# Kernel tuning notes

Hardware: AMD Instinct MI355X
Metric: run time of the kernel (lower is better)

## Reference

```python
import jax, jax.numpy as jnp
import numpy as np

B, N, C = 8, 4096, 512

def setup_inputs() -> dict:
    key = jax.random.key(0)
    ks = jax.random.split(key, 6)
    s = 1.0 / np.sqrt(C)
    return {
        "x": jax.random.normal(ks[0], (B, N, C), jnp.float32),
        "Wq": jax.random.normal(ks[1], (C, C), jnp.float32) * s,
        "Wk": jax.random.normal(ks[2], (C, C), jnp.float32) * s,
        "Wv": jax.random.normal(ks[3], (C, C), jnp.float32) * s,
        "W1": jax.random.normal(ks[4], (C, C), jnp.float32) * s,
        "W2": jax.random.normal(ks[5], (C, C), jnp.float32) * s,
    }

def reference(x, Wq, Wk, Wv, W1, W2):
    # torch nn.Linear: y = x @ W.T (bias=False)
    q = x @ Wq.T                      # [B,N,C]
    k = x @ Wk.T
    v = x @ Wv.T
    dim = q.shape[-1]
    q = jax.nn.softmax(q, axis=-1) * (dim ** -0.5)   # softmax over channels
    k = jax.nn.softmax(k, axis=-2)                   # softmax over sequence
    context = jnp.einsum('bnd,bne->bde', k, v)       # [B,C,C]
    attn = jnp.einsum('bnd,bde->bne', q, context)    # [B,N,C]
    x = attn + x
    return (x @ W1.T) @ W2.T + x
```

## Files before the change

### kernel.cpp

```cpp
#include <hip/hip_runtime.h>

typedef unsigned int uint;
typedef __bf16 bf16_t;
typedef bf16_t bf16x8 __attribute__((ext_vector_type(8)));
typedef float floatx4 __attribute__((ext_vector_type(4)));

struct __align__(8) us4 { unsigned short x, y, z, w; };

__device__ __forceinline__ unsigned short f2b(float f) {
    unsigned u = __float_as_uint(f);
    u = u + 0x7FFFu + ((u >> 16) & 1u);
    return (unsigned short)(u >> 16);
}
__device__ __forceinline__ float b2f(unsigned short h) {
    return __uint_as_float(((unsigned)h) << 16);
}

__device__ __forceinline__ void g2l16(const void* g, void* l) {
    __builtin_amdgcn_global_load_lds((__attribute__((address_space(1))) void*)g,
                                     (__attribute__((address_space(3))) void*)l,
                                     16, 0, 0);
}

__device__ __forceinline__ float wave_max(float v) {
#pragma unroll
    for (int m = 32; m > 0; m >>= 1) v = fmaxf(v, __shfl_xor(v, m));
    return v;
}
__device__ __forceinline__ float wave_sum(float v) {
#pragma unroll
    for (int m = 32; m > 0; m >>= 1) v += __shfl_xor(v, m);
    return v;
}

template <int MODE, int NT, bool BMS>
__global__ __launch_bounds__(256, 4) void gemm128s(
    const unsigned short* __restrict__ A, const unsigned short* __restrict__ B,
    void* __restrict__ O, const unsigned short* __restrict__ R,
    unsigned short* __restrict__ O2, unsigned short* __restrict__ O3,
    int K, int lda, int ldb, int ldo, long long sB)
{
    __shared__ __attribute__((aligned(16))) unsigned short As[128 * 32];
    __shared__ __attribute__((aligned(16))) unsigned short Bs[128 * 32];

    const uint id = blockIdx.x;
    const uint xcd = id & 7;
    const uint g = id >> 3;
    const uint nt = g % NT;
    const uint mg = g / NT;
    const uint ms = mg * 8 + xcd;

    int bb, arow0;
    if constexpr (BMS) { bb = ms & 7; arow0 = bb * 4096 + (int)(ms >> 3) * 128; }
    else               { bb = 0;      arow0 = (int)ms * 128; }
    const int n0 = (int)nt * 128;

    const unsigned short* Bb = B + (long long)bb * sB;
    const int tid = threadIdx.x;
    const int l = tid & 63;
    const int w = tid >> 6;
    const int wm = (w >> 1) * 64;
    const int wn = (w & 1) * 64;

    const int srow = tid >> 2;
    const int scol = (tid & 3) * 8;
    const unsigned short* ga = A + (long long)(arow0 + srow) * lda + scol;
    const unsigned short* gb = Bb + (long long)(n0 + srow) * ldb + scol;
    unsigned short* la = As + tid * 8;
    unsigned short* lb = Bs + tid * 8;

    const int fr = l & 15;
    const int kq = (l >> 4) * 8;

    floatx4 acc[4][4] = {};

    for (int kt = 0; kt < K; kt += 32) {
        __syncthreads();
        g2l16(ga, la);
        g2l16(ga + (long long)64 * lda, la + 64 * 32);
        g2l16(gb, lb);
        g2l16(gb + (long long)64 * ldb, lb + 64 * 32);
        ga += 32; gb += 32;
        __syncthreads();

        bf16x8 af[4], bfr[4];
#pragma unroll
        for (int i = 0; i < 4; ++i) {
            af[i]  = *(const bf16x8*)(As + (wm + i * 16 + fr) * 32 + kq);
            bfr[i] = *(const bf16x8*)(Bs + (wn + i * 16 + fr) * 32 + kq);
        }
#pragma unroll
        for (int i = 0; i < 4; ++i)
#pragma unroll
            for (int j = 0; j < 4; ++j)
                acc[i][j] = __builtin_amdgcn_mfma_f32_16x16x32_bf16(
                    af[i], bfr[j], acc[i][j], 0, 0, 0);
    }

    const int col = l & 15;
    const int rbase = (l >> 4) * 4;

    if constexpr (MODE == 4) {
        if (n0 < 512) {
            unsigned short* Oq = (unsigned short*)O;
#pragma unroll
            for (int i = 0; i < 4; ++i)
#pragma unroll
                for (int j = 0; j < 4; ++j) {
                    int gn = n0 + wn + j * 16 + col;
                    int gmb = arow0 + wm + i * 16 + rbase;
#pragma unroll
                    for (int r = 0; r < 4; ++r)
                        Oq[(long long)(gmb + r) * 512 + gn] = f2b(acc[i][j][r]);
                }
        } else {
            unsigned short* T = (n0 < 1024) ? O2 : O3;
            const int nbase = (n0 < 1024) ? 512 : 1024;
            const int b = arow0 >> 12;
            const int mq0 = arow0 & 4095;
#pragma unroll
            for (int i = 0; i < 4; ++i)
#pragma unroll
                for (int j = 0; j < 4; ++j) {
                    int gn = n0 + wn + j * 16 + col - nbase;
                    int mq = mq0 + wm + i * 16 + rbase;
                    us4 pk = { f2b(acc[i][j][0]), f2b(acc[i][j][1]),
                               f2b(acc[i][j][2]), f2b(acc[i][j][3]) };
                    *(us4*)(T + ((long long)b * 512 + gn) * 4096 + mq) = pk;
                }
        }
    } else {
#pragma unroll
        for (int i = 0; i < 4; ++i)
#pragma unroll
            for (int j = 0; j < 4; ++j) {
                int gn = n0 + wn + j * 16 + col;
                int gmb = arow0 + wm + i * 16 + rbase;
#pragma unroll
                for (int r = 0; r < 4; ++r) {
                    long long idx = (long long)(gmb + r) * ldo + gn;
                    float v = acc[i][j][r];
                    if constexpr (MODE == 0) {
                        ((unsigned short*)O)[idx] = f2b(v);
                    } else if constexpr (MODE == 2) {
                        ((unsigned short*)O)[idx] = f2b(v + b2f(R[idx]));
                    } else {
                        ((float*)O)[idx] = v + b2f(R[idx]);
                    }
                }
            }
    }
}

__global__ __launch_bounds__(256, 4) void ctx_gemm_sk(
    const unsigned short* __restrict__ V, const unsigned short* __restrict__ Kt,
    float* __restrict__ P)
{
    __shared__ __attribute__((aligned(16))) unsigned short As[128 * 32];
    __shared__ __attribute__((aligned(16))) unsigned short Bs[128 * 32];

    const uint id = blockIdx.x;
    const uint xcd = id & 7;
    const uint g = id >> 3;
    const uint sub = g & 15;
    const int z = (int)(g >> 4) * 8 + (int)xcd;
    const int b = z >> 2;
    const int s = z & 3;
    const int m0 = (int)(sub >> 2) * 128;
    const int n0 = (int)(sub & 3) * 128;

    const unsigned short* Ab = V  + (long long)b * 512 * 4096 + s * 1024;
    const unsigned short* Bb = Kt + (long long)b * 512 * 4096 + s * 1024;

    const int tid = threadIdx.x;
    const int l = tid & 63;
    const int w = tid >> 6;
    const int wm = (w >> 1) * 64;
    const int wn = (w & 1) * 64;

    const int srow = tid >> 2;
    const int scol = (tid & 3) * 8;
    const unsigned short* ga = Ab + (long long)(m0 + srow) * 4096 + scol;
    const unsigned short* gb = Bb + (long long)(n0 + srow) * 4096 + scol;
    unsigned short* la = As + tid * 8;
    unsigned short* lb = Bs + tid * 8;

    const int fr = l & 15;
    const int kq = (l >> 4) * 8;

    floatx4 acc[4][4] = {};

    for (int kt = 0; kt < 1024; kt += 32) {
        __syncthreads();
        g2l16(ga, la);
        g2l16(ga + (long long)64 * 4096, la + 64 * 32);
        g2l16(gb, lb);
        g2l16(gb + (long long)64 * 4096, lb + 64 * 32);
        ga += 32; gb += 32;
        __syncthreads();

        bf16x8 af[4], bfr[4];
#pragma unroll
        for (int i = 0; i < 4; ++i) {
            af[i]  = *(const bf16x8*)(As + (wm + i * 16 + fr) * 32 + kq);
            bfr[i] = *(const bf16x8*)(Bs + (wn + i * 16 + fr) * 32 + kq);
        }
#pragma unroll
        for (int i = 0; i < 4; ++i)
#pragma unroll
            for (int j = 0; j < 4; ++j)
                acc[i][j] = __builtin_amdgcn_mfma_f32_16x16x32_bf16(
                    af[i], bfr[j], acc[i][j], 0, 0, 0);
    }

    const int col = l & 15;
    const int rbase = (l >> 4) * 4;
    float* Pb = P + ((long long)z * 16 + (sub >> 2) * 4 + (sub & 3)) * 16384;
#pragma unroll
    for (int i = 0; i < 4; ++i)
#pragma unroll
        for (int j = 0; j < 4; ++j)
#pragma unroll
            for (int r = 0; r < 4; ++r)
                Pb[(wm + i * 16 + rbase + r) * 128 + wn + j * 16 + col] =
                    acc[i][j][r];
}

__global__ __launch_bounds__(256) void ctx_reduce(const float* __restrict__ P,
                                                  unsigned short* __restrict__ Ct)
{
    long long f = (long long)blockIdx.x * 256 + threadIdx.x;
    long long base = f * 4;
    int tile = (int)(base >> 14);
    int lo = (int)(base & 16383);
    int b = tile >> 4;
    int mt = (tile >> 2) & 3;
    int nt = tile & 3;
    float4 s = {0.f, 0.f, 0.f, 0.f};
#pragma unroll
    for (int sp = 0; sp < 4; ++sp) {
        float4 v = *(const float4*)(P + ((long long)(b * 4 + sp) * 16 + mt * 4 + nt) * 16384 + lo);
        s.x += v.x; s.y += v.y; s.z += v.z; s.w += v.w;
    }
    int le = lo >> 7;
    int ld = lo & 127;
    us4 o = { f2b(s.x), f2b(s.y), f2b(s.z), f2b(s.w) };
    *(us4*)(Ct + (long long)b * 262144 + (mt * 128 + le) * 512 + nt * 128 + ld) = o;
}

__global__ __launch_bounds__(256) void f32_to_bf16_k(const float* __restrict__ in,
                                                     unsigned short* __restrict__ out)
{
    long long i = ((long long)blockIdx.x * 256 + threadIdx.x) * 4;
    float4 v = *(const float4*)(in + i);
    us4 o = { f2b(v.x), f2b(v.y), f2b(v.z), f2b(v.w) };
    *(us4*)(out + i) = o;
}

struct WPtrs { const float* in[5]; unsigned short* out[5]; };
__global__ __launch_bounds__(256) void conv_weights(WPtrs p)
{
    int which = blockIdx.y;
    long long i = ((long long)blockIdx.x * 256 + threadIdx.x) * 4;
    float4 v = *(const float4*)(p.in[which] + i);
    us4 o = { f2b(v.x), f2b(v.y), f2b(v.z), f2b(v.w) };
    *(us4*)(p.out[which] + i) = o;
}

__global__ __launch_bounds__(256) void softmax_row512(unsigned short* __restrict__ q,
                                                      float scale)
{
    __shared__ float red[8];
    unsigned short* p = q + (long long)blockIdx.x * 512;
    int t = threadIdx.x;
    uint v = *(const uint*)(p + 2 * t);
    float a = b2f((unsigned short)(v & 0xffff));
    float b = b2f((unsigned short)(v >> 16));
    float mx = wave_max(fmaxf(a, b));
    int w = t >> 6;
    if ((t & 63) == 0) red[w] = mx;
    __syncthreads();
    mx = fmaxf(fmaxf(red[0], red[1]), fmaxf(red[2], red[3]));
    float ea = __expf(a - mx), eb = __expf(b - mx);
    float s = wave_sum(ea + eb);
    if ((t & 63) == 0) red[4 + w] = s;
    __syncthreads();
    s = red[4] + red[5] + red[6] + red[7];
    float inv = scale / s;
    uint o = (uint)f2b(ea * inv) | ((uint)f2b(eb * inv) << 16);
    *(uint*)(p + 2 * t) = o;
}

__global__ __launch_bounds__(256) void softmax_row4096(unsigned short* __restrict__ kk)
{
    __shared__ float red[8];
    unsigned short* p = kk + (long long)blockIdx.x * 4096;
    int t = threadIdx.x;
    uint4 v0 = *(const uint4*)(p + 16 * t);
    uint4 v1 = *(const uint4*)(p + 16 * t + 8);
    uint u[8] = { v0.x, v0.y, v0.z, v0.w, v1.x, v1.y, v1.z, v1.w };
    float f[16];
#pragma unroll
    for (int i = 0; i < 8; ++i) {
        f[2 * i]     = b2f((unsigned short)(u[i] & 0xffff));
        f[2 * i + 1] = b2f((unsigned short)(u[i] >> 16));
    }
    float mx = f[0];
#pragma unroll
    for (int i = 1; i < 16; ++i) mx = fmaxf(mx, f[i]);
    mx = wave_max(mx);
    int w = t >> 6;
    if ((t & 63) == 0) red[w] = mx;
    __syncthreads();
    mx = fmaxf(fmaxf(red[0], red[1]), fmaxf(red[2], red[3]));
    float s = 0.f;
#pragma unroll
    for (int i = 0; i < 16; ++i) { f[i] = __expf(f[i] - mx); s += f[i]; }
    s = wave_sum(s);
    if ((t & 63) == 0) red[4 + w] = s;
    __syncthreads();
    s = red[4] + red[5] + red[6] + red[7];
    float inv = 1.f / s;
    uint o[8];
#pragma unroll
    for (int i = 0; i < 8; ++i)
        o[i] = (uint)f2b(f[2 * i] * inv) | ((uint)f2b(f[2 * i + 1] * inv) << 16);
    *(uint4*)(p + 16 * t)     = make_uint4(o[0], o[1], o[2], o[3]);
    *(uint4*)(p + 16 * t + 8) = make_uint4(o[4], o[5], o[6], o[7]);
}

extern "C" void kernel_launch(void* const* d_in, const int* in_sizes, int n_in,
                              void* d_out, int out_size, void* d_ws, size_t ws_size,
                              hipStream_t stream)
{
    (void)in_sizes; (void)n_in; (void)out_size; (void)ws_size;
    const float* x  = (const float*)d_in[0];
    const float* Wq = (const float*)d_in[1];
    const float* Wk = (const float*)d_in[2];
    const float* Wv = (const float*)d_in[3];
    const float* W1 = (const float*)d_in[4];
    const float* W2 = (const float*)d_in[5];
    float* out = (float*)d_out;

    const int Bn = 8, N = 4096, C = 512;
    const long long M  = (long long)Bn * N;
    const long long XE = M * C;

    char* ws = (char*)d_ws;
    size_t off = 0;
    auto carve = [&](size_t bytes) -> void* {
        void* p = ws + off;
        off += (bytes + 255) & ~(size_t)255;
        return p;
    };

    unsigned short* xb   = (unsigned short*)carve(XE * 2);
    unsigned short* wcat = (unsigned short*)carve((size_t)3 * C * C * 2);
    unsigned short* w1b  = (unsigned short*)carve((size_t)C * C * 2);
    unsigned short* w2b  = (unsigned short*)carve((size_t)C * C * 2);
    unsigned short* q    = (unsigned short*)carve(XE * 2);
    unsigned short* kT   = (unsigned short*)carve(XE * 2);
    unsigned short* vT   = (unsigned short*)carve(XE * 2);
    unsigned short* ctxT = (unsigned short*)carve((size_t)Bn * C * C * 2);
    unsigned short* xr = kT;
    unsigned short* h  = vT;
    float* P = (float*)d_out;

    f32_to_bf16_k<<<dim3((unsigned)(XE / 1024)), dim3(256), 0, stream>>>(x, xb);
    WPtrs wp = { { Wq, Wk, Wv, W1, W2 },
                 { wcat, wcat + C * C, wcat + 2 * C * C, w1b, w2b } };
    conv_weights<<<dim3((C * C) / 1024, 5), dim3(256), 0, stream>>>(wp);

    gemm128s<4, 12, false><<<dim3(3072), 256, 0, stream>>>(
        xb, wcat, q, nullptr, kT, vT, C, C, C, C, 0);

    softmax_row512<<<dim3((unsigned)M), 256, 0, stream>>>(q, 0.044194173824159216f);
    softmax_row4096<<<dim3(Bn * C), 256, 0, stream>>>(kT);

    ctx_gemm_sk<<<dim3(512), 256, 0, stream>>>(vT, kT, P);
    ctx_reduce<<<dim3(2048), 256, 0, stream>>>(P, ctxT);

    gemm128s<2, 4, true><<<dim3(1024), 256, 0, stream>>>(
        q, ctxT, xr, xb, nullptr, nullptr, C, C, C, C, (long long)C * C);

    gemm128s<0, 4, false><<<dim3(1024), 256, 0, stream>>>(
        xr, w1b, h, nullptr, nullptr, nullptr, C, C, C, C, 0);

    gemm128s<3, 4, false><<<dim3(1024), 256, 0, stream>>>(
        h, w2b, out, xr, nullptr, nullptr, C, C, C, C, 0);
}
```

Measured before the change: 344.2 us.

## Fuse softmaxes into QKV GEMM epilogue with deferred normalization; use K-tile 64

```diff
diff --git a/kernel.cpp b/kernel.cpp
--- a/kernel.cpp
+++ b/kernel.cpp
@@ -22,26 +22,17 @@
                                      16, 0, 0);
 }
 
-__device__ __forceinline__ float wave_max(float v) {
-#pragma unroll
-    for (int m = 32; m > 0; m >>= 1) v = fmaxf(v, __shfl_xor(v, m));
-    return v;
-}
-__device__ __forceinline__ float wave_sum(float v) {
-#pragma unroll
-    for (int m = 32; m > 0; m >>= 1) v += __shfl_xor(v, m);
-    return v;
-}
-
 template <int MODE, int NT, bool BMS>
-__global__ __launch_bounds__(256, 4) void gemm128s(
+__global__ __launch_bounds__(256, 4) void gemm64(
     const unsigned short* __restrict__ A, const unsigned short* __restrict__ B,
     void* __restrict__ O, const unsigned short* __restrict__ R,
     unsigned short* __restrict__ O2, unsigned short* __restrict__ O3,
-    int K, int lda, int ldb, int ldo, long long sB)
-{
-    __shared__ __attribute__((aligned(16))) unsigned short As[128 * 32];
-    __shared__ __attribute__((aligned(16))) unsigned short Bs[128 * 32];
+    float* __restrict__ Sq, float* __restrict__ Sk,
+    const float* __restrict__ Sn,
+    int K, int lda, int ldb, int ldo, long long sB, float scale)
+{
+    __shared__ __attribute__((aligned(16))) unsigned short As[128 * 64];
+    __shared__ __attribute__((aligned(16))) unsigned short Bs[128 * 64];
 
     const uint id = blockIdx.x;
     const uint xcd = id & 7;
@@ -62,8 +53,8 @@
     const int wm = (w >> 1) * 64;
     const int wn = (w & 1) * 64;
 
-    const int srow = tid >> 2;
-    const int scol = (tid & 3) * 8;
+    const int srow = tid >> 3;
+    const int scol = (tid & 7) * 8;
     const unsigned short* ga = A + (long long)(arow0 + srow) * lda + scol;
     const unsigned short* gb = Bb + (long long)(n0 + srow) * ldb + scol;
     unsigned short* la = As + tid * 8;
@@ -74,27 +65,31 @@
 
     floatx4 acc[4][4] = {};
 
-    for (int kt = 0; kt < K; kt += 32) {
+    for (int kt = 0; kt < K; kt += 64) {
         __syncthreads();
-        g2l16(ga, la);
-        g2l16(ga + (long long)64 * lda, la + 64 * 32);
-        g2l16(gb, lb);
-        g2l16(gb + (long long)64 * ldb, lb + 64 * 32);
-        ga += 32; gb += 32;
+#pragma unroll
+        for (int c = 0; c < 4; ++c) {
+            g2l16(ga + (long long)(c * 32) * lda, la + c * 2048);
+            g2l16(gb + (long long)(c * 32) * ldb, lb + c * 2048);
+        }
+        ga += 64; gb += 64;
         __syncthreads();
 
-        bf16x8 af[4], bfr[4];
-#pragma unroll
-        for (int i = 0; i < 4; ++i) {
-            af[i]  = *(const bf16x8*)(As + (wm + i * 16 + fr) * 32 + kq);
-            bfr[i] = *(const bf16x8*)(Bs + (wn + i * 16 + fr) * 32 + kq);
-        }
-#pragma unroll
-        for (int i = 0; i < 4; ++i)
-#pragma unroll
-            for (int j = 0; j < 4; ++j)
-                acc[i][j] = __builtin_amdgcn_mfma_f32_16x16x32_bf16(
-                    af[i], bfr[j], acc[i][j], 0, 0, 0);
+#pragma unroll
+        for (int h = 0; h < 2; ++h) {
+            bf16x8 af[4], bfr[4];
+#pragma unroll
+            for (int i = 0; i < 4; ++i) {
+                af[i]  = *(const bf16x8*)(As + (wm + i * 16 + fr) * 64 + kq + 32 * h);
+                bfr[i] = *(const bf16x8*)(Bs + (wn + i * 16 + fr) * 64 + kq + 32 * h);
+            }
+#pragma unroll
+            for (int i = 0; i < 4; ++i)
+#pragma unroll
+                for (int j = 0; j < 4; ++j)
+                    acc[i][j] = __builtin_amdgcn_mfma_f32_16x16x32_bf16(
+                        af[i], bfr[j], acc[i][j], 0, 0, 0);
+        }
     }
 
     const int col = l & 15;
@@ -103,6 +98,11 @@
     if constexpr (MODE == 4) {
         if (n0 < 512) {
             unsigned short* Oq = (unsigned short*)O;
+            float rs[4][4];
+#pragma unroll
+            for (int i = 0; i < 4; ++i)
+#pragma unroll
+                for (int r = 0; r < 4; ++r) rs[i][r] = 0.f;
 #pragma unroll
             for (int i = 0; i < 4; ++i)
 #pragma unroll
@@ -110,24 +110,81 @@
                     int gn = n0 + wn + j * 16 + col;
                     int gmb = arow0 + wm + i * 16 + rbase;
 #pragma unroll
-                    for (int r = 0; r < 4; ++r)
-                        Oq[(long long)(gmb + r) * 512 + gn] = f2b(acc[i][j][r]);
-                }
-        } else {
-            unsigned short* T = (n0 < 1024) ? O2 : O3;
-            const int nbase = (n0 < 1024) ? 512 : 1024;
+                    for (int r = 0; r < 4; ++r) {
+                        float e = __expf(acc[i][j][r]);
+                        rs[i][r] += e;
+                        Oq[(long long)(gmb + r) * 512 + gn] = f2b(e);
+                    }
+                }
+#pragma unroll
+            for (int i = 0; i < 4; ++i)
+#pragma unroll
+                for (int r = 0; r < 4; ++r) {
+                    float v = rs[i][r];
+                    v += __shfl_xor(v, 1);
+                    v += __shfl_xor(v, 2);
+                    v += __shfl_xor(v, 4);
+                    v += __shfl_xor(v, 8);
+                    if ((l & 15) == 0)
+                        atomicAdd(&Sq[arow0 + wm + i * 16 + rbase + r], v);
+                }
+        } else if (n0 < 1024) {
             const int b = arow0 >> 12;
             const int mq0 = arow0 & 4095;
+            float cs[4] = {0.f, 0.f, 0.f, 0.f};
 #pragma unroll
             for (int i = 0; i < 4; ++i)
 #pragma unroll
                 for (int j = 0; j < 4; ++j) {
-                    int gn = n0 + wn + j * 16 + col - nbase;
+                    int d = n0 + wn + j * 16 + col - 512;
+                    int mq = mq0 + wm + i * 16 + rbase;
+                    float e0 = __expf(acc[i][j][0]);
+                    float e1 = __expf(acc[i][j][1]);
+                    float e2 = __expf(acc[i][j][2]);
+                    float e3 = __expf(acc[i][j][3]);
+                    cs[j] += e0 + e1 + e2 + e3;
+                    us4 pk = { f2b(e0), f2b(e1), f2b(e2), f2b(e3) };
+                    *(us4*)(O2 + ((long long)b * 512 + d) * 4096 + mq) = pk;
+                }
+#pragma unroll
+            for (int j = 0; j < 4; ++j) {
+                float v = cs[j];
+                v += __shfl_xor(v, 16);
+                v += __shfl_xor(v, 32);
+                if (l < 16)
+                    atomicAdd(&Sk[b * 512 + n0 + wn + j * 16 + col - 512], v);
+            }
+        } else {
+            const int b = arow0 >> 12;
+            const int mq0 = arow0 & 4095;
+#pragma unroll
+            for (int i = 0; i < 4; ++i)
+#pragma unroll
+                for (int j = 0; j < 4; ++j) {
+                    int e = n0 + wn + j * 16 + col - 1024;
                     int mq = mq0 + wm + i * 16 + rbase;
                     us4 pk = { f2b(acc[i][j][0]), f2b(acc[i][j][1]),
                                f2b(acc[i][j][2]), f2b(acc[i][j][3]) };
-                    *(us4*)(T + ((long long)b * 512 + gn) * 4096 + mq) = pk;
-                }
+                    *(us4*)(O3 + ((long long)b * 512 + e) * 4096 + mq) = pk;
+                }
+        }
+    } else if constexpr (MODE == 5) {
+#pragma unroll
+        for (int i = 0; i < 4; ++i) {
+            int gmb = arow0 + wm + i * 16 + rbase;
+            float invs[4];
+#pragma unroll
+            for (int r = 0; r < 4; ++r) invs[r] = scale / Sn[gmb + r];
+#pragma unroll
+            for (int j = 0; j < 4; ++j) {
+                int gn = n0 + wn + j * 16 + col;
+#pragma unroll
+                for (int r = 0; r < 4; ++r) {
+                    long long idx = (long long)(gmb + r) * ldo + gn;
+                    ((unsigned short*)O)[idx] =
+                        f2b(acc[i][j][r] * invs[r] + b2f(R[idx]));
+                }
+            }
         }
     } else {
 #pragma unroll
@@ -142,8 +199,6 @@
                     float v = acc[i][j][r];
                     if constexpr (MODE == 0) {
                         ((unsigned short*)O)[idx] = f2b(v);
-                    } else if constexpr (MODE == 2) {
-                        ((unsigned short*)O)[idx] = f2b(v + b2f(R[idx]));
                     } else {
                         ((float*)O)[idx] = v + b2f(R[idx]);
                     }
@@ -156,8 +211,8 @@
     const unsigned short* __restrict__ V, const unsigned short* __restrict__ Kt,
     float* __restrict__ P)
 {
-    __shared__ __attribute__((aligned(16))) unsigned short As[128 * 32];
-    __shared__ __attribute__((aligned(16))) unsigned short Bs[128 * 32];
+    __shared__ __attribute__((aligned(16))) unsigned short As[128 * 64];
+    __shared__ __attribute__((aligned(16))) unsigned short Bs[128 * 64];
 
     const uint id = blockIdx.x;
     const uint xcd = id & 7;
@@ -178,8 +233,8 @@
     const int wm = (w >> 1) * 64;
     const int wn = (w & 1) * 64;
 
-    const int srow = tid >> 2;
-    const int scol = (tid & 3) * 8;
+    const int srow = tid >> 3;
+    const int scol = (tid & 7) * 8;
     const unsigned short* ga = Ab + (long long)(m0 + srow) * 4096 + scol;
     const unsigned short* gb = Bb + (long long)(n0 + srow) * 4096 + scol;
     unsigned short* la = As + tid * 8;
@@ -190,27 +245,31 @@
 
     floatx4 acc[4][4] = {};
 
-    for (int kt = 0; kt < 1024; kt += 32) {
+    for (int kt = 0; kt < 1024; kt += 64) {
         __syncthreads();
-        g2l16(ga, la);
-        g2l16(ga + (long long)64 * 4096, la + 64 * 32);
-        g2l16(gb, lb);
-        g2l16(gb + (long long)64 * 4096, lb + 64 * 32);
-        ga += 32; gb += 32;
+#pragma unroll
+        for (int c = 0; c < 4; ++c) {
+            g2l16(ga + (long long)(c * 32) * 4096, la + c * 2048);
+            g2l16(gb + (long long)(c * 32) * 4096, lb + c * 2048);
+        }
+        ga += 64; gb += 64;
         __syncthreads();
 
-        bf16x8 af[4], bfr[4];
-#pragma unroll
-        for (int i = 0; i < 4; ++i) {
-            af[i]  = *(const bf16x8*)(As + (wm + i * 16 + fr) * 32 + kq);
-            bfr[i] = *(const bf16x8*)(Bs + (wn + i * 16 + fr) * 32 + kq);
-        }
-#pragma unroll
-        for (int i = 0; i < 4; ++i)
-#pragma unroll
-            for (int j = 0; j < 4; ++j)
-                acc[i][j] = __builtin_amdgcn_mfma_f32_16x16x32_bf16(
-                    af[i], bfr[j], acc[i][j], 0, 0, 0);
+#pragma unroll
+        for (int h = 0; h < 2; ++h) {
+            bf16x8 af[4], bfr[4];
+#pragma unroll
+            for (int i = 0; i < 4; ++i) {
+                af[i]  = *(const bf16x8*)(As + (wm + i * 16 + fr) * 64 + kq + 32 * h);
+                bfr[i] = *(const bf16x8*)(Bs + (wn + i * 16 + fr) * 64 + kq + 32 * h);
+            }
+#pragma unroll
+            for (int i = 0; i < 4; ++i)
+#pragma unroll
+                for (int j = 0; j < 4; ++j)
+                    acc[i][j] = __builtin_amdgcn_mfma_f32_16x16x32_bf16(
+                        af[i], bfr[j], acc[i][j], 0, 0, 0);
+        }
     }
 
     const int col = l & 15;
@@ -227,6 +286,7 @@
 }
 
 __global__ __launch_bounds__(256) void ctx_reduce(const float* __restrict__ P,
+                                                  const float* __restrict__ Sk,
                                                   unsigned short* __restrict__ Ct)
 {
     long long f = (long long)blockIdx.x * 256 + threadIdx.x;
@@ -244,7 +304,8 @@
     }
     int le = lo >> 7;
     int ld = lo & 127;
-    us4 o = { f2b(s.x), f2b(s.y), f2b(s.z), f2b(s.w) };
+    float4 sk = *(const float4*)(Sk + b * 512 + nt * 128 + ld);
+    us4 o = { f2b(s.x / sk.x), f2b(s.y / sk.y), f2b(s.z / sk.z), f2b(s.w / sk.w) };
     *(us4*)(Ct + (long long)b * 262144 + (mt * 128 + le) * 512 + nt * 128 + ld) = o;
 }
 
@@ -267,66 +328,10 @@
     *(us4*)(p.out[which] + i) = o;
 }
 
-__global__ __launch_bounds__(256) void softmax_row512(unsigned short* __restrict__ q,
-                                                      float scale)
-{
-    __shared__ float red[8];
-    unsigned short* p = q + (long long)blockIdx.x * 512;
-    int t = threadIdx.x;
-    uint v = *(const uint*)(p + 2 * t);
-    float a = b2f((unsigned short)(v & 0xffff));
-    float b = b2f((unsigned short)(v >> 16));
-    float mx = wave_max(fmaxf(a, b));
-    int w = t >> 6;
-    if ((t & 63) == 0) red[w] = mx;
-    __syncthreads();
-    mx = fmaxf(fmaxf(red[0], red[1]), fmaxf(red[2], red[3]));
-    float ea = __expf(a - mx), eb = __expf(b - mx);
-    float s = wave_sum(ea + eb);
-    if ((t & 63) == 0) red[4 + w] = s;
-    __syncthreads();
-    s = red[4] + red[5] + red[6] + red[7];
-    float inv = scale / s;
-    uint o = (uint)f2b(ea * inv) | ((uint)f2b(eb * inv) << 16);
-    *(uint*)(p + 2 * t) = o;
-}
-
-__global__ __launch_bounds__(256) void softmax_row4096(unsigned short* __restrict__ kk)
-{
-    __shared__ float red[8];
-    unsigned short* p = kk + (long long)blockIdx.x * 4096;
-    int t = threadIdx.x;
-    uint4 v0 = *(const uint4*)(p + 16 * t);
-    uint4 v1 = *(const uint4*)(p + 16 * t + 8);
-    uint u[8] = { v0.x, v0.y, v0.z, v0.w, v1.x, v1.y, v1.z, v1.w };
-    float f[16];
-#pragma unroll
-    for (int i = 0; i < 8; ++i) {
-        f[2 * i]     = b2f((unsigned short)(u[i] & 0xffff));
-        f[2 * i + 1] = b2f((unsigned short)(u[i] >> 16));
-    }
-    float mx = f[0];
-#pragma unroll
-    for (int i = 1; i < 16; ++i) mx = fmaxf(mx, f[i]);
-    mx = wave_max(mx);
-    int w = t >> 6;
-    if ((t & 63) == 0) red[w] = mx;
-    __syncthreads();
-    mx = fmaxf(fmaxf(red[0], red[1]), fmaxf(red[2], red[3]));
-    float s = 0.f;
-#pragma unroll
-    for (int i = 0; i < 16; ++i) { f[i] = __expf(f[i] - mx); s += f[i]; }
-    s = wave_sum(s);
-    if ((t & 63) == 0) red[4 + w] = s;
-    __syncthreads();
-    s = red[4] + red[5] + red[6] + red[7];
-    float inv = 1.f / s;
-    uint o[8];
-#pragma unroll
-    for (int i = 0; i < 8; ++i)
-        o[i] = (uint)f2b(f[2 * i] * inv) | ((uint)f2b(f[2 * i + 1] * inv) << 16);
-    *(uint4*)(p + 16 * t)     = make_uint4(o[0], o[1], o[2], o[3]);
-    *(uint4*)(p + 16 * t + 8) = make_uint4(o[4], o[5], o[6], o[7]);
+__global__ __launch_bounds__(256) void zero_f32(float* __restrict__ p)
+{
+    long long i = ((long long)blockIdx.x * 256 + threadIdx.x) * 4;
+    *(float4*)(p + i) = make_float4(0.f, 0.f, 0.f, 0.f);
 }
 
 extern "C" void kernel_launch(void* const* d_in, const int* in_sizes, int n_in,
@@ -362,30 +367,35 @@
     unsigned short* kT   = (unsigned short*)carve(XE * 2);
     unsigned short* vT   = (unsigned short*)carve(XE * 2);
     unsigned short* ctxT = (unsigned short*)carve((size_t)Bn * C * C * 2);
+    float* Ssum = (float*)carve((size_t)(M + Bn * C) * 4);
+    float* Sq = Ssum;
+    float* Sk = Ssum + M;
     unsigned short* xr = kT;
     unsigned short* h  = vT;
     float* P = (float*)d_out;
+
+    zero_f32<<<dim3(36), 256, 0, stream>>>(Ssum);
 
     f32_to_bf16_k<<<dim3((unsigned)(XE / 1024)), dim3(256), 0, stream>>>(x, xb);
     WPtrs wp = { { Wq, Wk, Wv, W1, W2 },
                  { wcat, wcat + C * C, wcat + 2 * C * C, w1b, w2b } };
     conv_weights<<<dim3((C * C) / 1024, 5), dim3(256), 0, stream>>>(wp);
 
-    gemm128s<4, 12, false><<<dim3(3072), 256, 0, stream>>>(
-        xb, wcat, q, nullptr, kT, vT, C, C, C, C, 0);
-
-    softmax_row512<<<dim3((unsigned)M), 256, 0, stream>>>(q, 0.044194173824159216f);
-    softmax_row4096<<<dim3(Bn * C), 256, 0, stream>>>(kT);
+    gemm64<4, 12, false><<<dim3(3072), 256, 0, stream>>>(
+        xb, wcat, q, nullptr, kT, vT, Sq, Sk, nullptr, C, C, C, C, 0, 0.f);
 
     ctx_gemm_sk<<<dim3(512), 256, 0, stream>>>(vT, kT, P);
-    ctx_reduce<<<dim3(2048), 256, 0, stream>>>(P, ctxT);
-
-    gemm128s<2, 4, true><<<dim3(1024), 256, 0, stream>>>(
-        q, ctxT, xr, xb, nullptr, nullptr, C, C, C, C, (long long)C * C);
-
-    gemm128s<0, 4, false><<<dim3(1024), 256, 0, stream>>>(
-        xr, w1b, h, nullptr, nullptr, nullptr, C, C, C, C, 0);
-
-    gemm128s<3, 4, false><<<dim3(1024), 256, 0, stream>>>(
-        h, w2b, out, xr, nullptr, nullptr, C, C, C, C, 0);
-}
+    ctx_reduce<<<dim3(2048), 256, 0, stream>>>(P, Sk, ctxT);
+
+    gemm64<5, 4, true><<<dim3(1024), 256, 0, stream>>>(
+        q, ctxT, xr, xb, nullptr, nullptr, nullptr, nullptr, Sq,
+        C, C, C, C, (long long)C * C, 0.044194173824159216f);
+
+    gemm64<0, 4, false><<<dim3(1024), 256, 0, stream>>>(
+        xr, w1b, h, nullptr, nullptr, nullptr, nullptr, nullptr, nullptr,
+        C, C, C, C, 0, 0.f);
+
+    gemm64<3, 4, false><<<dim3(1024), 256, 0, stream>>>(
+        h, w2b, out, xr, nullptr, nullptr, nullptr, nullptr, nullptr,
+        C, C, C, C, 0, 0.f);
+}
```

New measurement: 311.2 us. 1.11x faster.
